# Kernel tuning notes

Hardware: AMD Instinct MI355X
Metric: run time of the kernel (lower is better)

Reference implementation:

```python
import jax, jax.numpy as jnp
import numpy as np

WIDTH = 8  # fixed-point fractional bits (init arg Width)


def quantizer(x, width=WIDTH):
    # Fixed-point quantization to `width` fractional bits, clipped to [-1, 1].
    scale = jnp.asarray(2.0 ** width, x.dtype)
    return jnp.clip(jnp.round(x * scale) / scale, -1.0, 1.0)


def setup_inputs() -> dict:
    key = jax.random.key(0)
    k1, k2, k3 = jax.random.split(key, 3)
    N, H, W, C = 32, 56, 56, 128
    KH, KW, F = 3, 3, 256
    OH, OW = H - KH + 1, W - KW + 1  # valid padding, stride 1
    x = jax.random.normal(k1, (N, H, W, C), dtype=jnp.float32) * 0.5
    kernels = jax.random.normal(k2, (KH, KW, C, F), dtype=jnp.float32) * 0.01
    bias = jax.random.normal(k3, (OH, OW, F), dtype=jnp.float32) * 0.01
    return {"x": x, "kernels": kernels, "bias": bias}


def reference(x, kernels, bias):
    # Method == 'Fixed': quantize input and kernels, valid conv, quantize output,
    # then per-position bias add + ReLU.
    xq = quantizer(x)
    wq = quantizer(kernels)
    out = jax.lax.conv_general_dilated(
        xq, wq,
        window_strides=(1, 1),
        padding="VALID",
        dimension_numbers=("NHWC", "HWIO", "NHWC"),
    )
    out = quantizer(out)
    return jax.nn.relu(out + bias[None, :, :, :])
```

## Files before the change

kernel.cpp:

```cpp
#include <hip/hip_runtime.h>
#include <hip/hip_bf16.h>
#include <stdint.h>
#include <stddef.h>


typedef float  f32x4  __attribute__((ext_vector_type(4)));
typedef short  bf16x8 __attribute__((ext_vector_type(8)));

#define N_IMG 32
#define H_IN 56
#define W_IN 56
#define C_IN 128
#define F_OUT 256
#define OHW 54
#define M_TOTAL (N_IMG * OHW * OHW)
#define BM 128
#define BN 256
#define BK 64
#define NTILES 18
#define A_BUF_SHORTS (BM * BK)
#define B_BUF_SHORTS (BN * BK)
#define A_BUF_BYTES (A_BUF_SHORTS * 2)
#define B_BUF_BYTES (B_BUF_SHORTS * 2)

__device__ __forceinline__ unsigned short quant_to_bf16(float x) {
    float a = rintf(x * 256.0f);
    a = fminf(fmaxf(a, -256.0f), 256.0f);
    float q = a * 0.00390625f;
    union { float f; unsigned int u; } cv; cv.f = q;
    return (unsigned short)(cv.u >> 16);
}

__device__ __forceinline__ void async_copy16(const unsigned short* g, unsigned short* l) {
    __builtin_amdgcn_global_load_lds(
        (const __attribute__((address_space(1))) unsigned int*)g,
        (__attribute__((address_space(3))) unsigned int*)l, 16, 0, 0);
}

__device__ __forceinline__ unsigned lds_off(const void* p) {
    return (unsigned)(uintptr_t)(__attribute__((address_space(3))) const void*)p;
}

__device__ __forceinline__ bf16x8 lds_read_b128(unsigned addr) {
    bf16x8 r;
    asm volatile("ds_read_b128 %0, %1" : "=v"(r) : "v"(addr));
    return r;
}

__global__ __launch_bounds__(256) void quant_x_kernel(
        const float* __restrict__ x, unsigned short* __restrict__ xq) {
    int i = (blockIdx.x * 256 + threadIdx.x) * 4;
    float4 v = *reinterpret_cast<const float4*>(x + i);
    ushort4 o;
    o.x = quant_to_bf16(v.x);
    o.y = quant_to_bf16(v.y);
    o.z = quant_to_bf16(v.z);
    o.w = quant_to_bf16(v.w);
    *reinterpret_cast<ushort4*>(xq + i) = o;
}

__global__ __launch_bounds__(256) void quant_w_kernel(
        const float* __restrict__ w, unsigned short* __restrict__ wp) {
    int idx = blockIdx.x * 256 + threadIdx.x;
    int c  = idx & 127;
    int f  = (idx >> 7) & 255;
    int kk = idx >> 15;
    wp[idx] = quant_to_bf16(w[(kk * C_IN + c) * F_OUT + f]);
}

__global__ __launch_bounds__(512, 2) void conv_kernel(
        const unsigned short* __restrict__ xq,
        const unsigned short* __restrict__ wp,
        const float* __restrict__ bias,
        float* __restrict__ out)
{
    __shared__ __attribute__((aligned(16))) unsigned short Alds[3][A_BUF_SHORTS];
    __shared__ __attribute__((aligned(16))) unsigned short Blds[3][B_BUF_SHORTS];

    const int tid  = threadIdx.x;
    const int lane = tid & 63;
    const int wave = tid >> 6;
    const int wr   = wave >> 2;
    const int wc   = wave & 3;
    const int m0   = blockIdx.x * BM;

    const int rowt = tid >> 3;
    const int c16  = tid & 7;
    const int sw   = c16 ^ (rowt & 7);
    const int dstc = tid & ~63;

    const unsigned short* a_src[2];
#pragma unroll
    for (int r = 0; r < 2; ++r) {
        int m = m0 + 64 * r + rowt;
        int n_img = m / (OHW * OHW);
        int rem   = m % (OHW * OHW);
        int oh = rem / OHW, ow = rem % OHW;
        a_src[r] = xq + (size_t)((n_img * H_IN + oh) * W_IN + ow) * C_IN + sw * 8;
    }
    const unsigned short* b_src[4];
#pragma unroll
    for (int r = 0; r < 4; ++r)
        b_src[r] = wp + (size_t)(64 * r + rowt) * C_IN + sw * 8;

    const int mr = lane & 15;
    const int lq = lane >> 4;
    unsigned a_rd[4][2], b_rd[4][2];
    const unsigned Abase = lds_off(&Alds[0][0]);
    const unsigned Bbase = lds_off(&Blds[0][0]);
#pragma unroll
    for (int mi = 0; mi < 4; ++mi)
#pragma unroll
        for (int ks = 0; ks < 2; ++ks) {
            int row = wr * 64 + mi * 16 + mr;
            int ch  = (ks * 4 + lq) ^ (mr & 7);
            a_rd[mi][ks] = Abase + row * (BK * 2) + ch * 16;
        }
#pragma unroll
    for (int ni = 0; ni < 4; ++ni)
#pragma unroll
        for (int ks = 0; ks < 2; ++ks) {
            int row = wc * 64 + ni * 16 + mr;
            int ch  = (ks * 4 + lq) ^ (mr & 7);
            b_rd[ni][ks] = Bbase + row * (BK * 2) + ch * 16;
        }

    f32x4 acc[4][4];
#pragma unroll
    for (int i = 0; i < 4; ++i)
#pragma unroll
        for (int j = 0; j < 4; ++j) acc[i][j] = (f32x4)(0.0f);

    auto stage_p0 = [&](int tt, int bi) {
        int kk = tt >> 1, half = tt & 1;
        int kh = (kk * 43) >> 7, kw = kk - 3 * kh;
        int aoff = (kh * W_IN + kw) * C_IN + half * 64;
        int boff = kk * (F_OUT * C_IN) + half * 64;
        async_copy16(a_src[0] + aoff, &Alds[bi][dstc * 8]);
        async_copy16(a_src[1] + aoff, &Alds[bi][(512 + dstc) * 8]);
        async_copy16(b_src[0] + boff, &Blds[bi][dstc * 8]);
    };
    auto stage_p1 = [&](int tt, int bi) {
        int kk = tt >> 1, half = tt & 1;
        int boff = kk * (F_OUT * C_IN) + half * 64;
        async_copy16(b_src[1] + boff, &Blds[bi][(512 + dstc) * 8]);
        async_copy16(b_src[2] + boff, &Blds[bi][(1024 + dstc) * 8]);
        async_copy16(b_src[3] + boff, &Blds[bi][(1536 + dstc) * 8]);
    };

    auto do_tile = [&](int cur, int stage_tt, bool dostage, int endmode) {
        const unsigned ca = (unsigned)cur * A_BUF_BYTES;
        const unsigned cb = (unsigned)cur * B_BUF_BYTES;
        int bi = cur + 2; if (bi >= 3) bi -= 3;

        bf16x8 af[4][2], bq[2][2];
#pragma unroll
        for (int mi = 0; mi < 4; ++mi)
#pragma unroll
            for (int ks = 0; ks < 2; ++ks)
                af[mi][ks] = lds_read_b128(a_rd[mi][ks] + ca);
#pragma unroll
        for (int ni = 0; ni < 2; ++ni)
#pragma unroll
            for (int ks = 0; ks < 2; ++ks)
                bq[ni][ks] = lds_read_b128(b_rd[ni][ks] + cb);
        if (dostage) stage_p0(stage_tt, bi);
        asm volatile("" ::: "memory");
        __builtin_amdgcn_s_barrier();
        asm volatile("s_waitcnt lgkmcnt(0)" ::: "memory");
        __builtin_amdgcn_sched_barrier(0);
        __builtin_amdgcn_s_setprio(1);
#pragma unroll
        for (int mi = 0; mi < 4; ++mi)
#pragma unroll
            for (int ni = 0; ni < 2; ++ni)
#pragma unroll
                for (int ks = 0; ks < 2; ++ks)
                    acc[mi][ni] = __builtin_amdgcn_mfma_f32_16x16x32_bf16(
                        af[mi][ks], bq[ni][ks], acc[mi][ni], 0, 0, 0);
        __builtin_amdgcn_s_setprio(0);
        asm volatile("" ::: "memory");
        __builtin_amdgcn_s_barrier();

#pragma unroll
        for (int ni = 0; ni < 2; ++ni)
#pragma unroll
            for (int ks = 0; ks < 2; ++ks)
                bq[ni][ks] = lds_read_b128(b_rd[ni + 2][ks] + cb);
        if (dostage) stage_p1(stage_tt, bi);
        asm volatile("" ::: "memory");
        __builtin_amdgcn_s_barrier();
        asm volatile("s_waitcnt lgkmcnt(0)" ::: "memory");
        __builtin_amdgcn_sched_barrier(0);
        __builtin_amdgcn_s_setprio(1);
#pragma unroll
        for (int mi = 0; mi < 4; ++mi)
#pragma unroll
            for (int ni = 0; ni < 2; ++ni)
#pragma unroll
                for (int ks = 0; ks < 2; ++ks)
                    acc[mi][ni + 2] = __builtin_amdgcn_mfma_f32_16x16x32_bf16(
                        af[mi][ks], bq[ni][ks], acc[mi][ni + 2], 0, 0, 0);
        __builtin_amdgcn_s_setprio(0);
        if (endmode == 0)      asm volatile("s_waitcnt vmcnt(6)" ::: "memory");
        else if (endmode == 1) asm volatile("s_waitcnt vmcnt(0)" ::: "memory");
        if (endmode <= 1) {
            asm volatile("" ::: "memory");
            __builtin_amdgcn_s_barrier();
        }
    };

    stage_p0(0, 0); stage_p1(0, 0);
    stage_p0(1, 1); stage_p1(1, 1);
    asm volatile("s_waitcnt vmcnt(6)" ::: "memory");
    __builtin_amdgcn_s_barrier();

#pragma unroll 1
    for (int t = 0; t < 16; ++t) {
        int cur = t - (t / 3) * 3;
        do_tile(cur, t + 2, true, 0);
    }
    do_tile(1, 0, false, 1);
    do_tile(2, 0, false, 2);

    const int fcol0 = wc * 64 + mr;
#pragma unroll
    for (int mi = 0; mi < 4; ++mi) {
#pragma unroll
        for (int rr = 0; rr < 4; ++rr) {
            const int m = m0 + wr * 64 + mi * 16 + lq * 4 + rr;
            const float* brow = bias + (size_t)(m % (OHW * OHW)) * F_OUT;
            float* orow = out + (size_t)m * F_OUT;
#pragma unroll
            for (int ni = 0; ni < 4; ++ni) {
                float v = acc[mi][ni][rr];
                float t = rintf(v * 256.0f);
                t = fminf(fmaxf(t, -256.0f), 256.0f);
                float o = t * 0.00390625f + brow[fcol0 + ni * 16];
                orow[fcol0 + ni * 16] = fmaxf(o, 0.0f);
            }
        }
    }
}

extern "C" void kernel_launch(void* const* d_in, const int* in_sizes, int n_in,
                              void* d_out, int out_size, void* d_ws, size_t ws_size,
                              hipStream_t stream) {
    (void)in_sizes; (void)n_in; (void)out_size;
    const float* x    = (const float*)d_in[0];
    const float* w    = (const float*)d_in[1];
    const float* bias = (const float*)d_in[2];
    float* out        = (float*)d_out;

    const size_t x_elems = (size_t)N_IMG * H_IN * W_IN * C_IN;
    const size_t w_elems = (size_t)9 * F_OUT * C_IN;
    const size_t xq_bytes = x_elems * sizeof(unsigned short);
    const size_t need = xq_bytes + w_elems * sizeof(unsigned short);
    if (ws_size < need) return;

    unsigned short* xq = (unsigned short*)d_ws;
    unsigned short* wp = (unsigned short*)((char*)d_ws + xq_bytes);

    quant_x_kernel<<<(int)(x_elems / (256 * 4)), 256, 0, stream>>>(x, xq);
    quant_w_kernel<<<(int)(w_elems / 256), 256, 0, stream>>>(w, wp);
    conv_kernel<<<M_TOTAL / BM, 512, 0, stream>>>(xq, wp, bias, out);
}
```

Baseline: 94.98 us.

## Double M tile to 256 with double-buffered LDS and XCD-aware block remap

Doubles the conv GEMM M tile from 128 to 256 rows per block and uses two LDS buffers instead of three, each holding 256 A rows and 256 B rows. Each wave now computes an 8x4 grid of 16x16 MFMA accumulators, with B fragments for the next tile prefetched across the tile boundary. Block indices are remapped so consecutive M tiles land on the same XCD, and the last partial tile is clamped and guarded. This halves B (weight) reloads per output row and raises arithmetic intensity, but costs more accumulator registers and 128KB of LDS per block, which likely limits occupancy to one block per CU.

Result: slower. 123.9 us (+30.5%).

```diff
diff --git a/kernel.cpp b/kernel.cpp
--- a/kernel.cpp
+++ b/kernel.cpp
@@ -14,14 +14,10 @@
 #define F_OUT 256
 #define OHW 54
 #define M_TOTAL (N_IMG * OHW * OHW)
-#define BM 128
+#define BM 256
 #define BN 256
 #define BK 64
-#define NTILES 18
-#define A_BUF_SHORTS (BM * BK)
-#define B_BUF_SHORTS (BN * BK)
-#define A_BUF_BYTES (A_BUF_SHORTS * 2)
-#define B_BUF_BYTES (B_BUF_SHORTS * 2)
+#define NBLK ((M_TOTAL + BM - 1) / BM)
 
 __device__ __forceinline__ unsigned short quant_to_bf16(float x) {
     float a = rintf(x * 256.0f);
@@ -74,98 +70,92 @@
         const float* __restrict__ bias,
         float* __restrict__ out)
 {
-    __shared__ __attribute__((aligned(16))) unsigned short Alds[3][A_BUF_SHORTS];
-    __shared__ __attribute__((aligned(16))) unsigned short Blds[3][B_BUF_SHORTS];
+    __shared__ __attribute__((aligned(16))) unsigned short Alds[32768];
+    __shared__ __attribute__((aligned(16))) unsigned short Blds[32768];
 
     const int tid  = threadIdx.x;
     const int lane = tid & 63;
     const int wave = tid >> 6;
     const int wr   = wave >> 2;
     const int wc   = wave & 3;
-    const int m0   = blockIdx.x * BM;
+
+    int bid = blockIdx.x;
+    {
+        int xc = bid & 7, l = bid >> 3;
+        bid = (xc < 5 ? xc * 46 : 230 + (xc - 5) * 45) + l;
+    }
+    const int m0 = bid * BM;
 
     const int rowt = tid >> 3;
-    const int c16  = tid & 7;
-    const int sw   = c16 ^ (rowt & 7);
-    const int dstc = tid & ~63;
-
-    const unsigned short* a_src[2];
-#pragma unroll
-    for (int r = 0; r < 2; ++r) {
-        int m = m0 + 64 * r + rowt;
-        int n_img = m / (OHW * OHW);
-        int rem   = m % (OHW * OHW);
-        int oh = rem / OHW, ow = rem % OHW;
-        a_src[r] = xq + (size_t)((n_img * H_IN + oh) * W_IN + ow) * C_IN + sw * 8;
-    }
-    const unsigned short* b_src[4];
-#pragma unroll
-    for (int r = 0; r < 4; ++r)
-        b_src[r] = wp + (size_t)(64 * r + rowt) * C_IN + sw * 8;
+    const int sw   = (tid & 7) ^ (rowt & 7);
+    const int dstc = (tid & ~63) * 8;
+
+    const unsigned short* aP[4];
+#pragma unroll
+    for (int h = 0; h < 2; ++h)
+#pragma unroll
+        for (int r = 0; r < 2; ++r) {
+            int m = m0 + h * 128 + r * 64 + rowt;
+            if (m > M_TOTAL - 1) m = M_TOTAL - 1;
+            int n_img = m / (OHW * OHW);
+            int rem   = m % (OHW * OHW);
+            int oh = rem / OHW, ow = rem % OHW;
+            aP[h * 2 + r] = xq + (size_t)((n_img * H_IN + oh) * W_IN + ow) * C_IN + sw * 8;
+        }
+    const unsigned short* bP[4];
+#pragma unroll
+    for (int h = 0; h < 2; ++h)
+#pragma unroll
+        for (int r = 0; r < 2; ++r)
+            bP[h * 2 + r] = wp + (size_t)(h * 128 + r * 64 + rowt) * C_IN + sw * 8;
+
+    auto stageB = [&](int tt, int b) {
+        int kk = tt >> 1, hk = tt & 1;
+        int off = kk * (F_OUT * C_IN) + hk * 64;
+#pragma unroll
+        for (int h = 0; h < 2; ++h)
+#pragma unroll
+            for (int r = 0; r < 2; ++r)
+                async_copy16(bP[h * 2 + r] + off,
+                             Blds + (b * 2 + h) * 8192 + r * 4096 + dstc);
+    };
+    auto stageA = [&](int tt, int b) {
+        int kk = tt >> 1, hk = tt & 1;
+        int kh = (kk * 43) >> 7, kw = kk - 3 * kh;
+        int off = (kh * W_IN + kw) * C_IN + hk * 64;
+#pragma unroll
+        for (int h = 0; h < 2; ++h)
+#pragma unroll
+            for (int r = 0; r < 2; ++r)
+                async_copy16(aP[h * 2 + r] + off,
+                             Alds + (b * 2 + h) * 8192 + r * 4096 + dstc);
+    };
 
     const int mr = lane & 15;
     const int lq = lane >> 4;
-    unsigned a_rd[4][2], b_rd[4][2];
-    const unsigned Abase = lds_off(&Alds[0][0]);
-    const unsigned Bbase = lds_off(&Blds[0][0]);
-#pragma unroll
-    for (int mi = 0; mi < 4; ++mi)
-#pragma unroll
-        for (int ks = 0; ks < 2; ++ks) {
-            int row = wr * 64 + mi * 16 + mr;
-            int ch  = (ks * 4 + lq) ^ (mr & 7);
-            a_rd[mi][ks] = Abase + row * (BK * 2) + ch * 16;
-        }
-#pragma unroll
-    for (int ni = 0; ni < 4; ++ni)
-#pragma unroll
-        for (int ks = 0; ks < 2; ++ks) {
-            int row = wc * 64 + ni * 16 + mr;
-            int ch  = (ks * 4 + lq) ^ (mr & 7);
-            b_rd[ni][ks] = Bbase + row * (BK * 2) + ch * 16;
-        }
-
-    f32x4 acc[4][4];
-#pragma unroll
-    for (int i = 0; i < 4; ++i)
+    unsigned ch[2];
+    ch[0] = (unsigned)(((0 * 4 + lq) ^ (mr & 7)) * 16);
+    ch[1] = (unsigned)(((1 * 4 + lq) ^ (mr & 7)) * 16);
+    const unsigned aB0 = lds_off(Alds) + wr * 16384 + mr * 128;
+    const unsigned bB0 = lds_off(Blds) + (wc >> 1) * 16384 + ((wc & 1) * 64 + mr) * 128;
+
+    f32x4 acc[8][4];
+#pragma unroll
+    for (int i = 0; i < 8; ++i)
 #pragma unroll
         for (int j = 0; j < 4; ++j) acc[i][j] = (f32x4)(0.0f);
 
-    auto stage_p0 = [&](int tt, int bi) {
-        int kk = tt >> 1, half = tt & 1;
-        int kh = (kk * 43) >> 7, kw = kk - 3 * kh;
-        int aoff = (kh * W_IN + kw) * C_IN + half * 64;
-        int boff = kk * (F_OUT * C_IN) + half * 64;
-        async_copy16(a_src[0] + aoff, &Alds[bi][dstc * 8]);
-        async_copy16(a_src[1] + aoff, &Alds[bi][(512 + dstc) * 8]);
-        async_copy16(b_src[0] + boff, &Blds[bi][dstc * 8]);
-    };
-    auto stage_p1 = [&](int tt, int bi) {
-        int kk = tt >> 1, half = tt & 1;
-        int boff = kk * (F_OUT * C_IN) + half * 64;
-        async_copy16(b_src[1] + boff, &Blds[bi][(512 + dstc) * 8]);
-        async_copy16(b_src[2] + boff, &Blds[bi][(1024 + dstc) * 8]);
-        async_copy16(b_src[3] + boff, &Blds[bi][(1536 + dstc) * 8]);
-    };
-
-    auto do_tile = [&](int cur, int stage_tt, bool dostage, int endmode) {
-        const unsigned ca = (unsigned)cur * A_BUF_BYTES;
-        const unsigned cb = (unsigned)cur * B_BUF_BYTES;
-        int bi = cur + 2; if (bi >= 3) bi -= 3;
-
-        bf16x8 af[4][2], bq[2][2];
+    bf16x8 bfr[4][2];
+
+    auto do_tile = [&](int buf, int stage_tt, bool do_stage, bool read_next, int vm) {
+        const unsigned ab = aB0 + buf * 32768;
+        const unsigned bb = bB0 + buf * 32768;
+        bf16x8 af[4][2];
 #pragma unroll
         for (int mi = 0; mi < 4; ++mi)
 #pragma unroll
             for (int ks = 0; ks < 2; ++ks)
-                af[mi][ks] = lds_read_b128(a_rd[mi][ks] + ca);
-#pragma unroll
-        for (int ni = 0; ni < 2; ++ni)
-#pragma unroll
-            for (int ks = 0; ks < 2; ++ks)
-                bq[ni][ks] = lds_read_b128(b_rd[ni][ks] + cb);
-        if (dostage) stage_p0(stage_tt, bi);
-        asm volatile("" ::: "memory");
+                af[mi][ks] = lds_read_b128(ab + mi * 2048 + ch[ks]);
         __builtin_amdgcn_s_barrier();
         asm volatile("s_waitcnt lgkmcnt(0)" ::: "memory");
         __builtin_amdgcn_sched_barrier(0);
@@ -177,18 +167,14 @@
 #pragma unroll
                 for (int ks = 0; ks < 2; ++ks)
                     acc[mi][ni] = __builtin_amdgcn_mfma_f32_16x16x32_bf16(
-                        af[mi][ks], bq[ni][ks], acc[mi][ni], 0, 0, 0);
-        __builtin_amdgcn_s_setprio(0);
-        asm volatile("" ::: "memory");
-        __builtin_amdgcn_s_barrier();
-
+                        af[mi][ks], bfr[ni][ks], acc[mi][ni], 0, 0, 0);
+        __builtin_amdgcn_s_setprio(0);
+        __builtin_amdgcn_s_barrier();
 #pragma unroll
         for (int ni = 0; ni < 2; ++ni)
 #pragma unroll
             for (int ks = 0; ks < 2; ++ks)
-                bq[ni][ks] = lds_read_b128(b_rd[ni + 2][ks] + cb);
-        if (dostage) stage_p1(stage_tt, bi);
-        asm volatile("" ::: "memory");
+                bfr[2 + ni][ks] = lds_read_b128(bb + (2 + ni) * 2048 + ch[ks]);
         __builtin_amdgcn_s_barrier();
         asm volatile("s_waitcnt lgkmcnt(0)" ::: "memory");
         __builtin_amdgcn_sched_barrier(0);
@@ -199,45 +185,90 @@
             for (int ni = 0; ni < 2; ++ni)
 #pragma unroll
                 for (int ks = 0; ks < 2; ++ks)
-                    acc[mi][ni + 2] = __builtin_amdgcn_mfma_f32_16x16x32_bf16(
-                        af[mi][ks], bq[ni][ks], acc[mi][ni + 2], 0, 0, 0);
-        __builtin_amdgcn_s_setprio(0);
-        if (endmode == 0)      asm volatile("s_waitcnt vmcnt(6)" ::: "memory");
-        else if (endmode == 1) asm volatile("s_waitcnt vmcnt(0)" ::: "memory");
-        if (endmode <= 1) {
-            asm volatile("" ::: "memory");
-            __builtin_amdgcn_s_barrier();
+                    acc[mi][2 + ni] = __builtin_amdgcn_mfma_f32_16x16x32_bf16(
+                        af[mi][ks], bfr[2 + ni][ks], acc[mi][2 + ni], 0, 0, 0);
+        __builtin_amdgcn_s_setprio(0);
+        __builtin_amdgcn_s_barrier();
+#pragma unroll
+        for (int mi = 0; mi < 4; ++mi)
+#pragma unroll
+            for (int ks = 0; ks < 2; ++ks)
+                af[mi][ks] = lds_read_b128(ab + 8192 + mi * 2048 + ch[ks]);
+        if (do_stage) stageB(stage_tt, buf);
+        __builtin_amdgcn_s_barrier();
+        asm volatile("s_waitcnt lgkmcnt(0)" ::: "memory");
+        __builtin_amdgcn_sched_barrier(0);
+        __builtin_amdgcn_s_setprio(1);
+#pragma unroll
+        for (int mi = 0; mi < 4; ++mi)
+#pragma unroll
+            for (int ni = 0; ni < 2; ++ni)
+#pragma unroll
+                for (int ks = 0; ks < 2; ++ks)
+                    acc[4 + mi][ni] = __builtin_amdgcn_mfma_f32_16x16x32_bf16(
+                        af[mi][ks], bfr[ni][ks], acc[4 + mi][ni], 0, 0, 0);
+        __builtin_amdgcn_s_setprio(0);
+        __builtin_amdgcn_s_barrier();
+        if (vm == 4)      asm volatile("s_waitcnt vmcnt(4)" ::: "memory");
+        else if (vm == 0) asm volatile("s_waitcnt vmcnt(0)" ::: "memory");
+        if (vm >= 0) __builtin_amdgcn_s_barrier();
+        if (read_next) {
+            const unsigned bbn = bB0 + (buf ^ 1) * 32768;
+#pragma unroll
+            for (int ni = 0; ni < 2; ++ni)
+#pragma unroll
+                for (int ks = 0; ks < 2; ++ks)
+                    bfr[ni][ks] = lds_read_b128(bbn + ni * 2048 + ch[ks]);
         }
+        if (do_stage) stageA(stage_tt, buf);
+        __builtin_amdgcn_s_setprio(1);
+#pragma unroll
+        for (int mi = 0; mi < 4; ++mi)
+#pragma unroll
+            for (int ni = 0; ni < 2; ++ni)
+#pragma unroll
+                for (int ks = 0; ks < 2; ++ks)
+                    acc[4 + mi][2 + ni] = __builtin_amdgcn_mfma_f32_16x16x32_bf16(
+                        af[mi][ks], bfr[2 + ni][ks], acc[4 + mi][2 + ni], 0, 0, 0);
+        __builtin_amdgcn_s_setprio(0);
+        __builtin_amdgcn_s_barrier();
     };
 
-    stage_p0(0, 0); stage_p1(0, 0);
-    stage_p0(1, 1); stage_p1(1, 1);
-    asm volatile("s_waitcnt vmcnt(6)" ::: "memory");
+    stageB(0, 0); stageA(0, 0);
+    stageB(1, 1); stageA(1, 1);
+    asm volatile("s_waitcnt vmcnt(8)" ::: "memory");
     __builtin_amdgcn_s_barrier();
+#pragma unroll
+    for (int ni = 0; ni < 2; ++ni)
+#pragma unroll
+        for (int ks = 0; ks < 2; ++ks)
+            bfr[ni][ks] = lds_read_b128(bB0 + ni * 2048 + ch[ks]);
 
 #pragma unroll 1
-    for (int t = 0; t < 16; ++t) {
-        int cur = t - (t / 3) * 3;
-        do_tile(cur, t + 2, true, 0);
+    for (int tp = 0; tp < 8; ++tp) {
+        do_tile(0, 2 * tp + 2, true, true, 4);
+        do_tile(1, 2 * tp + 3, true, true, 4);
     }
-    do_tile(1, 0, false, 1);
-    do_tile(2, 0, false, 2);
-
-    const int fcol0 = wc * 64 + mr;
-#pragma unroll
-    for (int mi = 0; mi < 4; ++mi) {
+    do_tile(0, 0, false, true, 0);
+    do_tile(1, 0, false, false, -1);
+
+#pragma unroll
+    for (int mi = 0; mi < 8; ++mi) {
 #pragma unroll
         for (int rr = 0; rr < 4; ++rr) {
-            const int m = m0 + wr * 64 + mi * 16 + lq * 4 + rr;
-            const float* brow = bias + (size_t)(m % (OHW * OHW)) * F_OUT;
-            float* orow = out + (size_t)m * F_OUT;
-#pragma unroll
-            for (int ni = 0; ni < 4; ++ni) {
-                float v = acc[mi][ni][rr];
-                float t = rintf(v * 256.0f);
-                t = fminf(fmaxf(t, -256.0f), 256.0f);
-                float o = t * 0.00390625f + brow[fcol0 + ni * 16];
-                orow[fcol0 + ni * 16] = fmaxf(o, 0.0f);
+            const int m = m0 + wr * 128 + (mi >> 2) * 64 + (mi & 3) * 16 + lq * 4 + rr;
+            if (m < M_TOTAL) {
+                const float* brow = bias + (size_t)(m % (OHW * OHW)) * F_OUT;
+                float* orow = out + (size_t)m * F_OUT;
+#pragma unroll
+                for (int ni = 0; ni < 4; ++ni) {
+                    const int fc = wc * 64 + ni * 16 + mr;
+                    float v = acc[mi][ni][rr];
+                    float t = rintf(v * 256.0f);
+                    t = fminf(fmaxf(t, -256.0f), 256.0f);
+                    float o = t * 0.00390625f + brow[fc];
+                    orow[fc] = fmaxf(o, 0.0f);
+                }
             }
         }
     }
@@ -263,5 +294,5 @@
 
     quant_x_kernel<<<(int)(x_elems / (256 * 4)), 256, 0, stream>>>(x, xq);
     quant_w_kernel<<<(int)(w_elems / 256), 256, 0, stream>>>(w, wp);
-    conv_kernel<<<M_TOTAL / BM, 512, 0, stream>>>(xq, wp, bias, out);
-}
+    conv_kernel<<<NBLK, 512, 0, stream>>>(xq, wp, bias, out);
+}
```
